# Kernel tuning notes

Hardware: AMD Instinct MI355X
Metric: run time of the kernel (lower is better)

The kernel has to match this reference:

```python
import jax, jax.numpy as jnp
import numpy as np
import math

# ---- constants derived from PCF.__init__(nbbins=50, sigma=0.25, npoints=1024, n_rmax=5) ----
NBBINS = 50
SIGMA = 0.25
NPOINTS = 1024
N_RMAX = 5
RMAX = float(2.0 * np.sqrt(1.0 / (2.0 * np.sqrt(3.0) * NPOINTS)))
_STEP = N_RMAX / NBBINS
RS = np.array([(i + 1) * _STEP * RMAX for i in range(NBBINS)], dtype=np.float32)
AREA = np.array([math.pi * ((r + 0.5 * RMAX) ** 2 - max(0.0, r - 0.5 * RMAX) ** 2) for r in RS],
                dtype=np.float32)
GF = float(1.0 / (np.sqrt(math.pi) * SIGMA))


def _gaussian_kernel(x):
    return GF * jnp.exp(-(x * x) / (SIGMA * SIGMA))


def _perimeter_weight(x, y, rs):
    """x, y: [N] disk centers in [0,1]^2; rs: [B]. Returns [N, B] inverse in-domain perimeter fraction."""
    full = jnp.full((x.shape[0], rs.shape[0]), 2.0 * math.pi, dtype=x.dtype)

    def corr(full_angle, dx, dy):
        # dx, dy: [N] distance to a domain edge (as in the four blocks of perimeter_weight)
        mask = rs[None, :] > dx[:, None]                       # [N, B]
        alpha = jnp.arccos(jnp.clip(dx[:, None] / rs[None, :], -1.0, 1.0))
        sub = (jnp.minimum(alpha, jnp.arctan2(dy, dx)[:, None])
               + jnp.minimum(alpha, jnp.arctan2(1.0 - dy, dx)[:, None]))
        return full_angle - jnp.where(mask, sub, 0.0)

    full = corr(full, x, y)          # left edge
    full = corr(full, 1.0 - x, y)    # right edge
    full = corr(full, y, x)          # bottom edge
    full = corr(full, 1.0 - y, x)    # top edge
    peri = jnp.clip(full / (2.0 * math.pi), 0.0, 1.0)
    pos = peri > 0
    return jnp.where(pos, 1.0 / jnp.where(pos, peri, 1.0), 0.0)


def _disk_distance(pa, pb, rmax):
    """pa: [Na,3], pb: [Nb,3] disks (x, y, r) -> pairwise disk distance [Na, Nb] (repo utils.diskDistance)."""
    diff = pa[:, None, 0:2] - pb[None, :, 0:2]
    d = jnp.sqrt(jnp.sum(diff * diff, axis=-1))                # [Na, Nb]
    ra = pa[:, 2][:, None]
    rb = pb[None, :, 2]
    r1 = jnp.maximum(ra, rb)
    r2 = jnp.minimum(ra, rb)
    extent = jnp.maximum(d + r1 + r2, 2.0 * r1)
    overlap = jnp.clip(r1 + r2 - d, 0.0, None)
    return (extent - overlap + d + r1 - r2) / rmax


def _pcf_forward(disks_a, disks_b, same_category):
    rs = jnp.asarray(RS)
    area = jnp.asarray(AREA)
    na = disks_a.shape[0]
    nb = disks_b.shape[0]
    dist = _disk_distance(disks_a, disks_b, RMAX)              # [Na, Nb]
    # val[i, j, b] = gauss(rs_b / rmax - dist_ij)
    val = _gaussian_kernel(rs[None, None, :] / RMAX - dist[:, :, None])  # [Na, Nb, B]
    if same_category:
        # exclude self-pair j == i (torch.cat of slices around i)
        eye = jnp.eye(na, nb, dtype=val.dtype)
        val = val * (1.0 - eye)[:, :, None]
    contrib = jnp.sum(val, axis=1)                             # [Na, B]
    weights = _perimeter_weight(disks_a[:, 0], disks_a[:, 1], rs)  # [Na, B] (diskfact = 1/domainLength = 1)
    density = contrib * weights / area[None, :] / nb           # [Na, B]
    pcf_mean = jnp.sum(density, axis=0) / na                   # [B]
    pcf_lower = jnp.min(density, axis=0)
    pcf_upper = jnp.max(density, axis=0)
    pcf = jnp.stack([rs / RMAX, pcf_mean], axis=1)             # [B, 2]
    return pcf, pcf_lower, pcf_upper


def setup_inputs() -> dict:
    key = jax.random.key(0)
    ka, kb = jax.random.split(key)
    disks_a = jax.random.uniform(ka, (1024, 3), dtype=jnp.float32)
    disks_b = jax.random.uniform(kb, (1024, 3), dtype=jnp.float32)
    return {"disks_a": disks_a, "disks_b": disks_b, "same_category": 0}


def reference(disks_a, disks_b, same_category):
    return _pcf_forward(disks_a, disks_b, same_category)
```

## Files before the change

kernel.cpp:

```cpp
#include <hip/hip_runtime.h>
#include <math.h>

#define NB 50

__device__ __forceinline__ float dev_rmax() {
    return (float)(2.0 * sqrt(1.0 / (2.0 * sqrt(3.0) * 1024.0)));
}

__global__ void __launch_bounds__(256)
pcf_density_kernel(const float* __restrict__ da, const float* __restrict__ db,
                   const int* __restrict__ scp, float* __restrict__ dens,
                   int na, int nb)
{
    const float RMAX = dev_rmax();
    const float inv_rmax = 1.0f / RMAX;
    const int i    = blockIdx.x;
    const int tid  = threadIdx.x;
    const int lane = tid & 63;
    const int wave = tid >> 6;
    const int sc   = scp[0];

    __shared__ float list[256];
    __shared__ int   cnt;
    __shared__ float part[4 * NB];

    if (tid == 0) cnt = 0;
    __syncthreads();

    const float ax = da[3*i+0];
    const float ay = da[3*i+1];
    const float ar = da[3*i+2];

    const float binf = 0.1f * (float)(lane + 1);
    float accb = 0.0f;

    for (int base = 0; base < nb; base += 256) {
        const int j = base + tid;
        bool close = false;
        float dist = 0.0f;
        if (j < nb) {
            const float bx = db[3*j+0];
            const float by = db[3*j+1];
            const float br = db[3*j+2];
            const float dx = ax - bx;
            const float dy = ay - by;
            const float d  = sqrtf(dx*dx + dy*dy);
            const float r1 = fmaxf(ar, br);
            const float r2 = fminf(ar, br);
            const float extent  = fmaxf(d + r1 + r2, 2.0f*r1);
            const float overlap = fmaxf(r1 + r2 - d, 0.0f);
            dist = (extent - overlap + d + r1 - r2) * inv_rmax;
            close = (dist < 7.5f) && !((sc != 0) && (j == i));
        }
        const unsigned long long m = __ballot(close);
        const int total  = __popcll(m);
        const int prefix = __popcll(m & ((1ull << lane) - 1ull));
        int wbase = 0;
        if (lane == 0) wbase = atomicAdd(&cnt, total);
        wbase = __shfl(wbase, 0);
        if (close) list[wbase + prefix] = dist;
        __syncthreads();

        const int M = cnt;
        for (int k = wave; k < M; k += 4) {
            const float dl = list[k];
            const float x  = binf - dl;
            accb += __expf(-16.0f * x * x);
        }
        __syncthreads();
        if (tid == 0) cnt = 0;
        __syncthreads();
    }

    if (lane < NB) part[wave * NB + lane] = accb;
    __syncthreads();

    if (wave == 0 && lane < NB) {
        const float s = part[lane] + part[NB + lane] + part[2*NB + lane] + part[3*NB + lane];

        const float PI = 3.14159265358979323846f;
        const float GF = 1.0f / (sqrtf(PI) * 0.25f);
        const float rs = 0.1f * (float)(lane + 1) * RMAX;

        float full = 2.0f * PI;
        const float ex[4] = { ax, 1.0f - ax, ay, 1.0f - ay };
        const float ey[4] = { ay, ay,        ax, ax        };
#pragma unroll
        for (int c = 0; c < 4; ++c) {
            if (rs > ex[c]) {
                float ratio = ex[c] / rs;
                ratio = fminf(fmaxf(ratio, -1.0f), 1.0f);
                const float alpha = acosf(ratio);
                const float a1 = atan2f(ey[c], ex[c]);
                const float a2 = atan2f(1.0f - ey[c], ex[c]);
                full -= fminf(alpha, a1) + fminf(alpha, a2);
            }
        }
        float peri = full * (1.0f / (2.0f * PI));
        peri = fminf(fmaxf(peri, 0.0f), 1.0f);
        const float w = (peri > 0.0f) ? (1.0f / peri) : 0.0f;

        const float r_out = rs + 0.5f * RMAX;
        const float r_in  = fmaxf(rs - 0.5f * RMAX, 0.0f);
        const float area  = PI * (r_out * r_out - r_in * r_in);

        const float density = (GF * s) * w / area / (float)nb;
        dens[lane * na + i] = density;
    }
}

__global__ void __launch_bounds__(256)
pcf_reduce_kernel(const float* __restrict__ dens, float* __restrict__ out, int na)
{
    const int b    = blockIdx.x;
    const int tid  = threadIdx.x;
    const int lane = tid & 63;
    const int wave = tid >> 6;
    const float RMAX = dev_rmax();

    __shared__ float rs_[4], rmn[4], rmx[4];

    float s = 0.0f, mn = INFINITY, mx = -INFINITY;
    for (int i = tid; i < na; i += 256) {
        const float v = dens[b * na + i];
        s  += v;
        mn  = fminf(mn, v);
        mx  = fmaxf(mx, v);
    }
#pragma unroll
    for (int off = 32; off >= 1; off >>= 1) {
        s  += __shfl_down(s, off);
        mn  = fminf(mn, __shfl_down(mn, off));
        mx  = fmaxf(mx, __shfl_down(mx, off));
    }
    if (lane == 0) { rs_[wave] = s; rmn[wave] = mn; rmx[wave] = mx; }
    __syncthreads();
    if (tid == 0) {
        float ts = rs_[0] + rs_[1] + rs_[2] + rs_[3];
        float tmn = fminf(fminf(rmn[0], rmn[1]), fminf(rmn[2], rmn[3]));
        float tmx = fmaxf(fmaxf(rmx[0], rmx[1]), fmaxf(rmx[2], rmx[3]));
        const float rs = 0.1f * (float)(b + 1) * RMAX;
        out[2*b + 0] = rs / RMAX;
        out[2*b + 1] = ts / (float)na;
        out[100 + b] = tmn;
        out[150 + b] = tmx;
    }
}

extern "C" void kernel_launch(void* const* d_in, const int* in_sizes, int n_in,
                              void* d_out, int out_size, void* d_ws, size_t ws_size,
                              hipStream_t stream)
{
    const float* da = (const float*)d_in[0];
    const float* db = (const float*)d_in[1];
    const int*   sc = (const int*)d_in[2];
    float* out  = (float*)d_out;
    float* dens = (float*)d_ws;
    const int na = in_sizes[0] / 3;
    const int nb = in_sizes[1] / 3;

    pcf_density_kernel<<<na, 256, 0, stream>>>(da, db, sc, dens, na, nb);
    pcf_reduce_kernel<<<NB, 256, 0, stream>>>(dens, out, na);
}
```

Measured before the change: 63.88 us.

## Process all B disks in one chunk with squared-distance prefilter

Each block now handles 1024 B disks per iteration instead of 256, loading four per thread up front, so the synchronisation and list-reset rounds drop from four to one for nb=1024. A cheap squared-center-distance cutoff rejects far pairs before the sqrt and disk-distance maths. Survivors are appended to the shared list with a per-thread LDS atomic in place of the ballot/prefix compaction. This may add atomic contention on the counter and changes the order of list entries, which alters float summation order.

New measurement: 63.35 us, median of 2. Within noise of the previous version (-0.8%).

```diff
diff --git a/kernel.cpp b/kernel.cpp
--- a/kernel.cpp
+++ b/kernel.cpp
@@ -14,18 +14,18 @@
 {
     const float RMAX = dev_rmax();
     const float inv_rmax = 1.0f / RMAX;
+    const float dd_cut = (3.75f * RMAX) * (3.75f * RMAX);
     const int i    = blockIdx.x;
     const int tid  = threadIdx.x;
     const int lane = tid & 63;
     const int wave = tid >> 6;
     const int sc   = scp[0];
 
-    __shared__ float list[256];
+    __shared__ float list[1024];
     __shared__ int   cnt;
     __shared__ float part[4 * NB];
 
     if (tid == 0) cnt = 0;
-    __syncthreads();
 
     const float ax = da[3*i+0];
     const float ay = da[3*i+1];
@@ -34,42 +34,68 @@
     const float binf = 0.1f * (float)(lane + 1);
     float accb = 0.0f;
 
-    for (int base = 0; base < nb; base += 256) {
-        const int j = base + tid;
-        bool close = false;
-        float dist = 0.0f;
-        if (j < nb) {
-            const float bx = db[3*j+0];
-            const float by = db[3*j+1];
-            const float br = db[3*j+2];
-            const float dx = ax - bx;
-            const float dy = ay - by;
-            const float d  = sqrtf(dx*dx + dy*dy);
-            const float r1 = fmaxf(ar, br);
-            const float r2 = fminf(ar, br);
-            const float extent  = fmaxf(d + r1 + r2, 2.0f*r1);
-            const float overlap = fmaxf(r1 + r2 - d, 0.0f);
-            dist = (extent - overlap + d + r1 - r2) * inv_rmax;
-            close = (dist < 7.5f) && !((sc != 0) && (j == i));
+    __syncthreads();
+
+    for (int base = 0; base < nb; base += 1024) {
+        const int chunk = (nb - base < 1024) ? (nb - base) : 1024;
+        if (chunk == 1024) {
+            float bx[4], by[4], br[4];
+#pragma unroll
+            for (int k = 0; k < 4; ++k) {
+                const int j = base + tid + 256 * k;
+                bx[k] = db[3*j+0];
+                by[k] = db[3*j+1];
+                br[k] = db[3*j+2];
+            }
+#pragma unroll
+            for (int k = 0; k < 4; ++k) {
+                const int j = base + tid + 256 * k;
+                const float dx = ax - bx[k];
+                const float dy = ay - by[k];
+                const float dd = dx*dx + dy*dy;
+                if (dd < dd_cut && !((sc != 0) && (j == i))) {
+                    const float d  = sqrtf(dd);
+                    const float r1 = fmaxf(ar, br[k]);
+                    const float r2 = fminf(ar, br[k]);
+                    const float extent  = fmaxf(d + r1 + r2, 2.0f*r1);
+                    const float overlap = fmaxf(r1 + r2 - d, 0.0f);
+                    const float dist = (extent - overlap + d + r1 - r2) * inv_rmax;
+                    if (dist < 7.5f) list[atomicAdd(&cnt, 1)] = dist;
+                }
+            }
+        } else {
+            for (int jo = tid; jo < chunk; jo += 256) {
+                const int j = base + jo;
+                const float bx = db[3*j+0];
+                const float by = db[3*j+1];
+                const float br = db[3*j+2];
+                const float dx = ax - bx;
+                const float dy = ay - by;
+                const float dd = dx*dx + dy*dy;
+                if (dd < dd_cut && !((sc != 0) && (j == i))) {
+                    const float d  = sqrtf(dd);
+                    const float r1 = fmaxf(ar, br);
+                    const float r2 = fminf(ar, br);
+                    const float extent  = fmaxf(d + r1 + r2, 2.0f*r1);
+                    const float overlap = fmaxf(r1 + r2 - d, 0.0f);
+                    const float dist = (extent - overlap + d + r1 - r2) * inv_rmax;
+                    if (dist < 7.5f) list[atomicAdd(&cnt, 1)] = dist;
+                }
+            }
         }
-        const unsigned long long m = __ballot(close);
-        const int total  = __popcll(m);
-        const int prefix = __popcll(m & ((1ull << lane) - 1ull));
-        int wbase = 0;
-        if (lane == 0) wbase = atomicAdd(&cnt, total);
-        wbase = __shfl(wbase, 0);
-        if (close) list[wbase + prefix] = dist;
         __syncthreads();
 
         const int M = cnt;
         for (int k = wave; k < M; k += 4) {
-            const float dl = list[k];
-            const float x  = binf - dl;
+            const float x = binf - list[k];
             accb += __expf(-16.0f * x * x);
         }
-        __syncthreads();
-        if (tid == 0) cnt = 0;
-        __syncthreads();
+
+        if (base + 1024 < nb) {
+            __syncthreads();
+            if (tid == 0) cnt = 0;
+            __syncthreads();
+        }
     }
 
     if (lane < NB) part[wave * NB + lane] = accb;
```
